# Kernel optimization log

Hardware: AMD Instinct MI355X
Metric: run time of the kernel (lower is better)

The kernel has to match this reference:

```python
import jax, jax.numpy as jnp
import numpy as np

N_EMBD = 1024
N_HEAD = 16
HEAD_DIM = N_EMBD // N_HEAD
LN_EPS = 1e-5


def setup_inputs() -> dict:
    key = jax.random.key(0)
    ks = jax.random.split(key, 8)
    B, T, C = 4, 2048, N_EMBD
    s = lambda fan_in: 1.0 / np.sqrt(fan_in)
    return {
        'x': jax.random.normal(ks[0], (B, T, C), dtype=jnp.float32),
        'w_qkv': jax.random.normal(ks[1], (C, 3 * C), dtype=jnp.float32) * s(C),
        'b_qkv': jnp.zeros((3 * C,), dtype=jnp.float32),
        'ln1_g': jnp.ones((C,), dtype=jnp.float32),
        'ln1_b': jnp.zeros((C,), dtype=jnp.float32),
        'w_fc1': jax.random.normal(ks[2], (C, 4 * C), dtype=jnp.float32) * s(C),
        'b_fc1': jnp.zeros((4 * C,), dtype=jnp.float32),
        'w_fc2': jax.random.normal(ks[3], (4 * C, C), dtype=jnp.float32) * s(4 * C),
        'b_fc2': jnp.zeros((C,), dtype=jnp.float32),
        'ln2_g': jnp.ones((C,), dtype=jnp.float32),
        'ln2_b': jnp.zeros((C,), dtype=jnp.float32),
    }


def _layernorm(x, g, b):
    mu = jnp.mean(x, axis=-1, keepdims=True)
    var = jnp.mean(jnp.square(x - mu), axis=-1, keepdims=True)
    return (x - mu) * jax.lax.rsqrt(var + LN_EPS) * g + b


def _attention(x, w_qkv, b_qkv):
    B, T, C = x.shape
    qkv = x @ w_qkv + b_qkv                      # [B,T,3C]
    q, k, v = jnp.split(qkv, 3, axis=-1)
    q = q.reshape(B, T, N_HEAD, HEAD_DIM)
    k = k.reshape(B, T, N_HEAD, HEAD_DIM)
    v = v.reshape(B, T, N_HEAD, HEAD_DIM)
    scores = jnp.einsum('bqhd,bkhd->bhqk', q, k) / np.sqrt(HEAD_DIM).astype(np.float32)
    causal = jnp.tril(jnp.ones((T, T), dtype=bool))
    scores = jnp.where(causal, scores, -jnp.inf)
    attn = jax.nn.softmax(scores, axis=-1)       # [B,H,T,T]
    y = jnp.einsum('bhqk,bkhd->bqhd', attn, v)
    return y.reshape(B, T, C)


def reference(x, w_qkv, b_qkv, ln1_g, ln1_b, w_fc1, b_fc1, w_fc2, b_fc2, ln2_g, ln2_b):
    # Block: x = ln1(x + attn(x)); x = ln2(x + mlp(x))   (post-LN residual)
    x = _layernorm(x + _attention(x, w_qkv, b_qkv), ln1_g, ln1_b)
    h = jax.nn.gelu(x @ w_fc1 + b_fc1, approximate=False)
    mlp = h @ w_fc2 + b_fc2
    x = _layernorm(x + mlp, ln2_g, ln2_b)
    return x
```

## Files before the change

kernel.cpp:

```cpp
#include <hip/hip_runtime.h>
#include <cstdint>
#include <cstddef>

#define TB 4
#define TT 2048
#define TC 1024
#define NH 16
#define HD 64
#define MROWS (TB * TT)

typedef __bf16 bf16;
typedef unsigned short u16;
typedef __bf16 bf16x8 __attribute__((ext_vector_type(8)));
typedef float floatx4 __attribute__((ext_vector_type(4)));
typedef unsigned short ushort8 __attribute__((ext_vector_type(8)));
typedef unsigned short ushort4v __attribute__((ext_vector_type(4)));

#define LOG2E 1.4426950408889634f

static __device__ __forceinline__ u16 f2bfbits(float f) {
    bf16 b = (bf16)f;
    return __builtin_bit_cast(u16, b);
}

#if __has_builtin(__builtin_amdgcn_exp2f)
#define EXP2F(x) __builtin_amdgcn_exp2f(x)
#else
#define EXP2F(x) exp2f(x)
#endif

static __device__ __forceinline__ void gld_lds16(const u16* g, const u16* lds) {
    __builtin_amdgcn_global_load_lds(
        (const __attribute__((address_space(1))) unsigned int*)(uintptr_t)g,
        (__attribute__((address_space(3))) unsigned int*)(unsigned int)(uintptr_t)lds,
        16, 0, 0);
}

__global__ void cast_bf16_kernel(const float* __restrict__ in, u16* __restrict__ out, int n4) {
    int i = blockIdx.x * blockDim.x + threadIdx.x;
    if (i < n4) {
        float4 v = reinterpret_cast<const float4*>(in)[i];
        ushort4v o;
        o.x = f2bfbits(v.x); o.y = f2bfbits(v.y); o.z = f2bfbits(v.z); o.w = f2bfbits(v.w);
        reinterpret_cast<ushort4v*>(out)[i] = o;
    }
}

__global__ void transpose_cast_kernel(const float* __restrict__ in, u16* __restrict__ out,
                                      int K, int N) {
    __shared__ float tile[32][33];
    const int n0 = blockIdx.x * 32, k0 = blockIdx.y * 32;
    const int tx = threadIdx.x, ty = threadIdx.y;
    for (int r = 0; r < 32; r += 8)
        tile[ty + r][tx] = in[(size_t)(k0 + ty + r) * N + n0 + tx];
    __syncthreads();
    for (int r = 0; r < 32; r += 8)
        out[(size_t)(n0 + ty + r) * K + k0 + tx] = f2bfbits(tile[tx][ty + r]);
}

template <int GELU>
__global__ __launch_bounds__(256) void gemm_bt_kernel(
    const u16* __restrict__ A, const u16* __restrict__ Bt,
    const float* __restrict__ bias, u16* __restrict__ Cmat,
    int Nsz, int Ksz)
{
    __shared__ u16 As[128 * 64];
    __shared__ u16 Bs[128 * 64];
    const int tid  = threadIdx.x;
    const int wave = tid >> 6, lane = tid & 63;
    const int quad = lane >> 4, l16 = lane & 15;
    const int wm = (wave >> 1) * 64, wn = (wave & 1) * 64;
    const int m0 = blockIdx.y * 128, n0 = blockIdx.x * 128;

    const int srow = lane >> 3;
    const int scol = ((lane & 7) ^ srow) * 8;
    const u16* ap = A  + (size_t)(m0 + wave * 32 + srow) * Ksz + scol;
    const u16* bp = Bt + (size_t)(n0 + wave * 32 + srow) * Ksz + scol;
    const size_t dstep = (size_t)8 * Ksz;

    floatx4 acc[4][4];
#pragma unroll
    for (int i = 0; i < 4; i++)
#pragma unroll
        for (int j = 0; j < 4; j++)
            acc[i][j] = (floatx4){0.f, 0.f, 0.f, 0.f};

    const int l7 = l16 & 7;

    for (int k0 = 0; k0 < Ksz; k0 += 64) {
        __syncthreads();
#pragma unroll
        for (int d = 0; d < 4; d++) {
            gld_lds16(ap + d * dstep, As + (wave * 4 + d) * 512);
            gld_lds16(bp + d * dstep, Bs + (wave * 4 + d) * 512);
        }
        ap += 64; bp += 64;
        __syncthreads();

#pragma unroll
        for (int t = 0; t < 2; t++) {
            const int po = ((t * 4 + quad) ^ l7) * 8;
            bf16x8 af[4], bfr[4];
#pragma unroll
            for (int i = 0; i < 4; i++)
                af[i] = *reinterpret_cast<const bf16x8*>(As + (wm + i * 16 + l16) * 64 + po);
#pragma unroll
            for (int j = 0; j < 4; j++)
                bfr[j] = *reinterpret_cast<const bf16x8*>(Bs + (wn + j * 16 + l16) * 64 + po);
#pragma unroll
            for (int i = 0; i < 4; i++)
#pragma unroll
                for (int j = 0; j < 4; j++)
                    acc[i][j] = __builtin_amdgcn_mfma_f32_16x16x32_bf16(af[i], bfr[j], acc[i][j], 0, 0, 0);
        }
    }

#pragma unroll
    for (int i = 0; i < 4; i++) {
        const int row_base = m0 + wm + i * 16 + quad * 4;
#pragma unroll
        for (int j = 0; j < 4; j++) {
            const int col = n0 + wn + j * 16 + l16;
            const float bv = bias[col];
#pragma unroll
            for (int r = 0; r < 4; r++) {
                float v = acc[i][j][r] + bv;
                if (GELU) {
                    float u = v * (0.7978845608f + 0.0356774081f * v * v);
                    float e = EXP2F(u * (2.0f * LOG2E));
                    v = v - v * __builtin_amdgcn_rcpf(e + 1.0f);
                }
                Cmat[(size_t)(row_base + r) * Nsz + col] = f2bfbits(v);
            }
        }
    }
}

__global__ __launch_bounds__(256, 4) void attn_kernel(const u16* __restrict__ qkv,
                                                      u16* __restrict__ y)
{
    __shared__ u16 Ks[64 * 64];
    __shared__ u16 Vt[64 * 64];
    __shared__ u16 Pw[4][16 * 64];
    const int tid  = threadIdx.x;
    const int wave = tid >> 6, lane = tid & 63;
    const int quad = lane >> 4, l16 = lane & 15;
    const int l7   = l16 & 7;
    const int h = blockIdx.y, b = blockIdx.z;
    const int rowbase = b * TT;
    const int S3C = 3 * TC;

    const int srow = tid >> 3;
    const int kc8  = (tid & 7) * 8;
    const int pcK  = ((tid & 7) ^ (srow & 7)) * 8;
    const int pvb  = (srow + ((tid & 7) << 2)) & 31;
    const int pcr  = (quad ^ l7) * 8;
    unsigned int* const vtw = (unsigned int*)Vt;
    const int wavq = wave * 16 + l16;

    for (int pass = 0; pass < 2; pass++) {
        const int qt  = pass ? (31 - (int)blockIdx.x) : (int)blockIdx.x;
        const int q0b = qt * 64;
        const int q0w = q0b + wave * 16;
        const int kend = q0b + 64;

        bf16x8 qf0, qf1;
        {
            const u16* qrow = qkv + (size_t)(rowbase + q0w + l16) * S3C + h * HD + quad * 8;
            bf16x8 t0 = *reinterpret_cast<const bf16x8*>(qrow);
            bf16x8 t1 = *reinterpret_cast<const bf16x8*>(qrow + 32);
#pragma unroll
            for (int i = 0; i < 8; i++) {
                t0[i] = (bf16)((float)t0[i] * (0.125f * LOG2E));
                t1[i] = (bf16)((float)t1[i] * (0.125f * LOG2E));
            }
            qf0 = t0; qf1 = t1;
        }

        float m_s = -__builtin_inff(), l_s = 0.f;
        floatx4 o_acc[4];
#pragma unroll
        for (int n = 0; n < 4; n++) o_acc[n] = (floatx4){0.f, 0.f, 0.f, 0.f};

        ushort8 kr0, kr1, vr0, vr1;
        {
            const u16* kb = qkv + (size_t)(rowbase + srow) * S3C + TC + h * HD + kc8;
            kr0 = *reinterpret_cast<const ushort8*>(kb);
            kr1 = *reinterpret_cast<const ushort8*>(kb + (size_t)32 * S3C);
            const u16* vb = qkv + (size_t)(rowbase + 2 * srow) * S3C + 2 * TC + h * HD + kc8;
            vr0 = *reinterpret_cast<const ushort8*>(vb);
            vr1 = *reinterpret_cast<const ushort8*>(vb + S3C);
        }

        for (int k0 = 0; k0 < kend; k0 += 64) {
            __syncthreads();
            *reinterpret_cast<ushort8*>(Ks + srow * 64 + pcK)        = kr0;
            *reinterpret_cast<ushort8*>(Ks + (srow + 32) * 64 + pcK) = kr1;
#pragma unroll
            for (int j = 0; j < 8; j++) {
                unsigned int pk = (unsigned int)vr0[j] | ((unsigned int)vr1[j] << 16);
                vtw[(kc8 + j) * 32 + (pvb ^ (j << 2))] = pk;
            }
            __syncthreads();

            if (k0 + 64 < kend) {
                const int kn = k0 + 64;
                const u16* kb = qkv + (size_t)(rowbase + kn + srow) * S3C + TC + h * HD + kc8;
                kr0 = *reinterpret_cast<const ushort8*>(kb);
                kr1 = *reinterpret_cast<const ushort8*>(kb + (size_t)32 * S3C);
                const u16* vb = qkv + (size_t)(rowbase + kn + 2 * srow) * S3C + 2 * TC + h * HD + kc8;
                vr0 = *reinterpret_cast<const ushort8*>(vb);
                vr1 = *reinterpret_cast<const ushort8*>(vb + S3C);
            }

            floatx4 st[4];
#pragma unroll
            for (int t = 0; t < 4; t++) {
                const u16* krowp = Ks + (t * 16 + l16) * 64;
                bf16x8 ka  = *reinterpret_cast<const bf16x8*>(krowp + pcr);
                bf16x8 kb2 = *reinterpret_cast<const bf16x8*>(krowp + (pcr ^ 32));
                floatx4 s = (floatx4){0.f, 0.f, 0.f, 0.f};
                s = __builtin_amdgcn_mfma_f32_16x16x32_bf16(ka, qf0, s, 0, 0, 0);
                s = __builtin_amdgcn_mfma_f32_16x16x32_bf16(kb2, qf1, s, 0, 0, 0);
                st[t] = s;
            }
            float v[16];
            if (k0 == q0b) {
#pragma unroll
                for (int t = 0; t < 4; t++)
#pragma unroll
                    for (int r = 0; r < 4; r++)
                        v[t * 4 + r] = (t * 16 + quad * 4 + r > wavq) ? -__builtin_inff()
                                                                      : st[t][r];
            } else {
#pragma unroll
                for (int t = 0; t < 4; t++)
#pragma unroll
                    for (int r = 0; r < 4; r++)
                        v[t * 4 + r] = st[t][r];
            }
            float mx = v[0];
#pragma unroll
            for (int i = 1; i < 16; i++) mx = fmaxf(mx, v[i]);
            mx = fmaxf(mx, __shfl_xor(mx, 16));
            mx = fmaxf(mx, __shfl_xor(mx, 32));
            const float mnew  = fmaxf(m_s, mx);
            const float alpha = EXP2F(m_s - mnew);
            float rs = 0.f;
            u16* const pwb = Pw[wave] + l16 * 64;
#pragma unroll
            for (int t = 0; t < 4; t++) {
                float p0 = EXP2F(v[t * 4 + 0] - mnew);
                float p1 = EXP2F(v[t * 4 + 1] - mnew);
                float p2 = EXP2F(v[t * 4 + 2] - mnew);
                float p3 = EXP2F(v[t * 4 + 3] - mnew);
                rs += (p0 + p1) + (p2 + p3);
                ushort4v pk;
                pk.x = f2bfbits(p0); pk.y = f2bfbits(p1);
                pk.z = f2bfbits(p2); pk.w = f2bfbits(p3);
                *reinterpret_cast<ushort4v*>(
                    pwb + ((2 * t + (quad >> 1)) ^ l7) * 8 + (quad & 1) * 4) = pk;
            }
            rs += __shfl_xor(rs, 16);
            rs += __shfl_xor(rs, 32);
            l_s = l_s * alpha + rs;
            m_s = mnew;
#pragma unroll
            for (int n = 0; n < 4; n++) o_acc[n] *= alpha;

            bf16x8 pf0 = *reinterpret_cast<const bf16x8*>(pwb + pcr);
            bf16x8 pf1 = *reinterpret_cast<const bf16x8*>(pwb + (pcr ^ 32));
#pragma unroll
            for (int n = 0; n < 4; n++) {
                const int dr  = n * 16 + l16;
                const int pd0 = ((4 * (quad + 2 * n + (l16 >> 3))) & 31) ^ (l7 << 2);
                bf16x8 vf0 = *reinterpret_cast<const bf16x8*>(vtw + dr * 32 + pd0);
                bf16x8 vf1 = *reinterpret_cast<const bf16x8*>(vtw + dr * 32 + (pd0 ^ 16));
                o_acc[n] = __builtin_amdgcn_mfma_f32_16x16x32_bf16(vf0, pf0, o_acc[n], 0, 0, 0);
                o_acc[n] = __builtin_amdgcn_mfma_f32_16x16x32_bf16(vf1, pf1, o_acc[n], 0, 0, 0);
            }
        }

        const float li = 1.0f / l_s;
        u16* yrow = y + (size_t)(rowbase + q0w + l16) * TC + h * HD;
#pragma unroll
        for (int n = 0; n < 4; n++) {
            ushort4v ov;
            ov.x = f2bfbits(o_acc[n][0] * li);
            ov.y = f2bfbits(o_acc[n][1] * li);
            ov.z = f2bfbits(o_acc[n][2] * li);
            ov.w = f2bfbits(o_acc[n][3] * li);
            *reinterpret_cast<ushort4v*>(yrow + n * 16 + quad * 4) = ov;
        }
    }
}

template <typename AT, typename OT>
__global__ __launch_bounds__(256) void ln_kernel(
    const AT* __restrict__ a, const bf16* __restrict__ bres,
    const float* __restrict__ g, const float* __restrict__ be,
    OT* __restrict__ out)
{
    const int row = blockIdx.x;
    const int tid = threadIdx.x;
    const size_t base = (size_t)row * TC;
    float v[4];
    for (int i = 0; i < 4; i++) {
        const int c = tid + i * 256;
        v[i] = (float)a[base + c] + (float)bres[base + c];
    }
    float s  = v[0] + v[1] + v[2] + v[3];
    float sq = v[0]*v[0] + v[1]*v[1] + v[2]*v[2] + v[3]*v[3];
    for (int off = 32; off >= 1; off >>= 1) {
        s  += __shfl_xor(s, off, 64);
        sq += __shfl_xor(sq, off, 64);
    }
    __shared__ float red[8];
    const int wv = tid >> 6, lane = tid & 63;
    if (lane == 0) { red[wv] = s; red[4 + wv] = sq; }
    __syncthreads();
    s  = red[0] + red[1] + red[2] + red[3];
    sq = red[4] + red[5] + red[6] + red[7];
    const float mu   = s * (1.0f / TC);
    const float var  = sq * (1.0f / TC) - mu * mu;
    const float rsig = rsqrtf(var + 1e-5f);
    for (int i = 0; i < 4; i++) {
        const int c = tid + i * 256;
        out[base + c] = (OT)((v[i] - mu) * rsig * g[c] + be[c]);
    }
}

extern "C" void kernel_launch(void* const* d_in, const int* in_sizes, int n_in,
                              void* d_out, int out_size, void* d_ws, size_t ws_size,
                              hipStream_t stream)
{
    const float* x     = (const float*)d_in[0];
    const float* w_qkv = (const float*)d_in[1];
    const float* b_qkv = (const float*)d_in[2];
    const float* ln1_g = (const float*)d_in[3];
    const float* ln1_b = (const float*)d_in[4];
    const float* w_fc1 = (const float*)d_in[5];
    const float* b_fc1 = (const float*)d_in[6];
    const float* w_fc2 = (const float*)d_in[7];
    const float* b_fc2 = (const float*)d_in[8];
    const float* ln2_g = (const float*)d_in[9];
    const float* ln2_b = (const float*)d_in[10];
    float* out = (float*)d_out;

    char* ws = (char*)d_ws;
    const size_t MB = 1ull << 20;
    u16* xb    = (u16*)(ws + 0);
    u16* wqkvT = (u16*)(ws + 16 * MB);
    u16* wfc1T = (u16*)(ws + 22 * MB);
    u16* wfc2T = (u16*)(ws + 30 * MB);
    u16* qkv   = (u16*)(ws + 38 * MB);
    u16* yb    = (u16*)(ws + 86 * MB);
    u16* x1    = (u16*)(ws + 102 * MB);
    u16* hb    = (u16*)(ws + 118 * MB);
    u16* mlp   = (u16*)(ws + 38 * MB);

    cast_bf16_kernel<<<(MROWS * TC / 4 + 255) / 256, 256, 0, stream>>>(x, xb, MROWS * TC / 4);
    transpose_cast_kernel<<<dim3(3 * TC / 32, TC / 32), dim3(32, 8), 0, stream>>>(w_qkv, wqkvT, TC, 3 * TC);
    transpose_cast_kernel<<<dim3(4 * TC / 32, TC / 32), dim3(32, 8), 0, stream>>>(w_fc1, wfc1T, TC, 4 * TC);
    transpose_cast_kernel<<<dim3(TC / 32, 4 * TC / 32), dim3(32, 8), 0, stream>>>(w_fc2, wfc2T, 4 * TC, TC);

    gemm_bt_kernel<0><<<dim3(3 * TC / 128, MROWS / 128), 256, 0, stream>>>(
        xb, wqkvT, b_qkv, qkv, 3 * TC, TC);
    attn_kernel<<<dim3(16, NH, TB), 256, 0, stream>>>(qkv, yb);
    ln_kernel<float, bf16><<<MROWS, 256, 0, stream>>>(x, (const bf16*)yb, ln1_g, ln1_b, (bf16*)x1);
    gemm_bt_kernel<1><<<dim3(4 * TC / 128, MROWS / 128), 256, 0, stream>>>(
        (const u16*)x1, wfc1T, b_fc1, hb, 4 * TC, TC);
    gemm_bt_kernel<0><<<dim3(TC / 128, MROWS / 128), 256, 0, stream>>>(
        hb, wfc2T, b_fc2, mlp, TC, 4 * TC);
    ln_kernel<bf16, float><<<MROWS, 256, 0, stream>>>(
        (const bf16*)x1, (const bf16*)mlp, ln2_g, ln2_b, out);
}
```

Before: 495.5 us.

## Merge prep kernels, pack GEMM epilogue stores, double-buffer 128-row attention tiles

Four cast/transpose launches are merged into one prep kernel that dispatches on block index. The GEMM epilogue now exchanges values between lane pairs so each lane writes packed 32-bit bf16 pairs instead of scalar 16-bit stores. The attention kernel moves to 512 threads covering 128 query rows, with double-buffered K/V in LDS, one barrier per step, and separate thread halves for the K and V staging. Waves skip fully masked key tiles. The tradeoff is more LDS and fewer blocks, and waves in the same block do unequal amounts of causal work.

```diff
diff --git a/kernel.cpp b/kernel.cpp
--- a/kernel.cpp
+++ b/kernel.cpp
@@ -36,21 +36,30 @@
         16, 0, 0);
 }
 
-__global__ void cast_bf16_kernel(const float* __restrict__ in, u16* __restrict__ out, int n4) {
-    int i = blockIdx.x * blockDim.x + threadIdx.x;
-    if (i < n4) {
-        float4 v = reinterpret_cast<const float4*>(in)[i];
+__global__ __launch_bounds__(256) void prep_kernel(
+    const float* __restrict__ x, u16* __restrict__ xb,
+    const float* __restrict__ w_qkv, u16* __restrict__ wqkvT,
+    const float* __restrict__ w_fc1, u16* __restrict__ wfc1T,
+    const float* __restrict__ w_fc2, u16* __restrict__ wfc2T)
+{
+    const int tid = threadIdx.x;
+    int blk = blockIdx.x;
+    if (blk < 8192) {
+        const int i = blk * 256 + tid;
+        float4 v = reinterpret_cast<const float4*>(x)[i];
         ushort4v o;
         o.x = f2bfbits(v.x); o.y = f2bfbits(v.y); o.z = f2bfbits(v.z); o.w = f2bfbits(v.w);
-        reinterpret_cast<ushort4v*>(out)[i] = o;
-    }
-}
-
-__global__ void transpose_cast_kernel(const float* __restrict__ in, u16* __restrict__ out,
-                                      int K, int N) {
+        reinterpret_cast<ushort4v*>(xb)[i] = o;
+        return;
+    }
+    blk -= 8192;
+    const float* in; u16* out; int K, N, bx, by;
+    if (blk < 3072)      { in = w_qkv; out = wqkvT; K = TC;     N = 3 * TC; bx = blk % 96;  by = blk / 96; }
+    else if (blk < 7168) { blk -= 3072; in = w_fc1; out = wfc1T; K = TC;    N = 4 * TC; bx = blk & 127; by = blk >> 7; }
+    else                 { blk -= 7168; in = w_fc2; out = wfc2T; K = 4 * TC; N = TC;    bx = blk & 31;  by = blk >> 5; }
     __shared__ float tile[32][33];
-    const int n0 = blockIdx.x * 32, k0 = blockIdx.y * 32;
-    const int tx = threadIdx.x, ty = threadIdx.y;
+    const int n0 = bx * 32, k0 = by * 32;
+    const int tx = tid & 31, ty = tid >> 5;
     for (int r = 0; r < 32; r += 8)
         tile[ty + r][tx] = in[(size_t)(k0 + ty + r) * N + n0 + tx];
     __syncthreads();
@@ -115,33 +124,48 @@
         }
     }
 
+    float bv[4];
+#pragma unroll
+    for (int j = 0; j < 4; j++) bv[j] = bias[n0 + wn + j * 16 + l16];
+    const int odd = l16 & 1;
 #pragma unroll
     for (int i = 0; i < 4; i++) {
-        const int row_base = m0 + wm + i * 16 + quad * 4;
+        const int row0 = m0 + wm + i * 16 + quad * 4;
 #pragma unroll
         for (int j = 0; j < 4; j++) {
-            const int col = n0 + wn + j * 16 + l16;
-            const float bv = bias[col];
+            float v[4];
 #pragma unroll
             for (int r = 0; r < 4; r++) {
-                float v = acc[i][j][r] + bv;
+                float t = acc[i][j][r] + bv[j];
                 if (GELU) {
-                    float u = v * (0.7978845608f + 0.0356774081f * v * v);
+                    float u = t * (0.7978845608f + 0.0356774081f * t * t);
                     float e = EXP2F(u * (2.0f * LOG2E));
-                    v = v - v * __builtin_amdgcn_rcpf(e + 1.0f);
-                }
-                Cmat[(size_t)(row_base + r) * Nsz + col] = f2bfbits(v);
+                    t = t - t * __builtin_amdgcn_rcpf(e + 1.0f);
+                }
+                v[r] = t;
             }
-        }
-    }
-}
-
-__global__ __launch_bounds__(256, 4) void attn_kernel(const u16* __restrict__ qkv,
-                                                      u16* __restrict__ y)
+            float pv0 = __shfl_xor(v[0], 1), pv1 = __shfl_xor(v[1], 1);
+            float pv2 = __shfl_xor(v[2], 1), pv3 = __shfl_xor(v[3], 1);
+            float lo0 = odd ? pv2 : v[0];
+            float hi0 = odd ? v[2] : pv0;
+            float lo1 = odd ? pv3 : v[1];
+            float hi1 = odd ? v[3] : pv1;
+            unsigned int d0 = (unsigned int)f2bfbits(lo0) | ((unsigned int)f2bfbits(hi0) << 16);
+            unsigned int d1 = (unsigned int)f2bfbits(lo1) | ((unsigned int)f2bfbits(hi1) << 16);
+            const int row  = row0 + odd * 2;
+            const int colp = n0 + wn + j * 16 + (l16 & ~1);
+            *reinterpret_cast<unsigned int*>(Cmat + (size_t)row * Nsz + colp)       = d0;
+            *reinterpret_cast<unsigned int*>(Cmat + (size_t)(row + 1) * Nsz + colp) = d1;
+        }
+    }
+}
+
+__global__ __launch_bounds__(512) void attn_kernel(const u16* __restrict__ qkv,
+                                                   u16* __restrict__ y)
 {
-    __shared__ u16 Ks[64 * 64];
-    __shared__ u16 Vt[64 * 64];
-    __shared__ u16 Pw[4][16 * 64];
+    __shared__ u16 Ks[2 * 64 * 64];
+    __shared__ u16 Vt[2 * 64 * 64];
+    __shared__ u16 Pw[8][16 * 64];
     const int tid  = threadIdx.x;
     const int wave = tid >> 6, lane = tid & 63;
     const int quad = lane >> 4, l16 = lane & 15;
@@ -150,19 +174,21 @@
     const int rowbase = b * TT;
     const int S3C = 3 * TC;
 
-    const int srow = tid >> 3;
-    const int kc8  = (tid & 7) * 8;
+    const int srow = (tid >> 3) & 31;
+    const int c8   = (tid & 7) * 8;
     const int pcK  = ((tid & 7) ^ (srow & 7)) * 8;
     const int pvb  = (srow + ((tid & 7) << 2)) & 31;
-    const int pcr  = (quad ^ l7) * 8;
+    const bool kRole = (tid < 256);
+    const int pcr = (quad ^ l7) * 8;
     unsigned int* const vtw = (unsigned int*)Vt;
-    const int wavq = wave * 16 + l16;
 
     for (int pass = 0; pass < 2; pass++) {
-        const int qt  = pass ? (31 - (int)blockIdx.x) : (int)blockIdx.x;
-        const int q0b = qt * 64;
-        const int q0w = q0b + wave * 16;
-        const int kend = q0b + 64;
+        const int qt   = pass ? (15 - (int)blockIdx.x) : (int)blockIdx.x;
+        const int q0b  = qt * 128;
+        const int q0w  = q0b + wave * 16;
+        const int kend = q0b + 128;
+
+        __syncthreads();
 
         bf16x8 qf0, qf1;
         {
@@ -182,103 +208,107 @@
 #pragma unroll
         for (int n = 0; n < 4; n++) o_acc[n] = (floatx4){0.f, 0.f, 0.f, 0.f};
 
-        ushort8 kr0, kr1, vr0, vr1;
-        {
-            const u16* kb = qkv + (size_t)(rowbase + srow) * S3C + TC + h * HD + kc8;
-            kr0 = *reinterpret_cast<const ushort8*>(kb);
-            kr1 = *reinterpret_cast<const ushort8*>(kb + (size_t)32 * S3C);
-            const u16* vb = qkv + (size_t)(rowbase + 2 * srow) * S3C + 2 * TC + h * HD + kc8;
-            vr0 = *reinterpret_cast<const ushort8*>(vb);
-            vr1 = *reinterpret_cast<const ushort8*>(vb + S3C);
-        }
-
+        const u16* gp = kRole
+            ? qkv + (size_t)(rowbase + srow) * S3C + TC + h * HD + c8
+            : qkv + (size_t)(rowbase + 2 * srow) * S3C + 2 * TC + h * HD + c8;
+        const size_t g2 = kRole ? (size_t)32 * S3C : (size_t)S3C;
+        ushort8 r0 = *reinterpret_cast<const ushort8*>(gp);
+        ushort8 r1 = *reinterpret_cast<const ushort8*>(gp + g2);
+
+        int buf = 0;
         for (int k0 = 0; k0 < kend; k0 += 64) {
-            __syncthreads();
-            *reinterpret_cast<ushort8*>(Ks + srow * 64 + pcK)        = kr0;
-            *reinterpret_cast<ushort8*>(Ks + (srow + 32) * 64 + pcK) = kr1;
-#pragma unroll
-            for (int j = 0; j < 8; j++) {
-                unsigned int pk = (unsigned int)vr0[j] | ((unsigned int)vr1[j] << 16);
-                vtw[(kc8 + j) * 32 + (pvb ^ (j << 2))] = pk;
+            if (kRole) {
+                u16* kb = Ks + buf * 4096;
+                *reinterpret_cast<ushort8*>(kb + srow * 64 + pcK)        = r0;
+                *reinterpret_cast<ushort8*>(kb + (srow + 32) * 64 + pcK) = r1;
+            } else {
+                unsigned int* vb = vtw + buf * 2048;
+#pragma unroll
+                for (int j = 0; j < 8; j++) {
+                    unsigned int pk = (unsigned int)r0[j] | ((unsigned int)r1[j] << 16);
+                    vb[(c8 + j) * 32 + (pvb ^ (j << 2))] = pk;
+                }
             }
             __syncthreads();
 
             if (k0 + 64 < kend) {
-                const int kn = k0 + 64;
-                const u16* kb = qkv + (size_t)(rowbase + kn + srow) * S3C + TC + h * HD + kc8;
-                kr0 = *reinterpret_cast<const ushort8*>(kb);
-                kr1 = *reinterpret_cast<const ushort8*>(kb + (size_t)32 * S3C);
-                const u16* vb = qkv + (size_t)(rowbase + kn + 2 * srow) * S3C + 2 * TC + h * HD + kc8;
-                vr0 = *reinterpret_cast<const ushort8*>(vb);
-                vr1 = *reinterpret_cast<const ushort8*>(vb + S3C);
+                const u16* gn = gp + (size_t)(k0 + 64) * S3C;
+                r0 = *reinterpret_cast<const ushort8*>(gn);
+                r1 = *reinterpret_cast<const ushort8*>(gn + g2);
             }
 
-            floatx4 st[4];
-#pragma unroll
-            for (int t = 0; t < 4; t++) {
-                const u16* krowp = Ks + (t * 16 + l16) * 64;
-                bf16x8 ka  = *reinterpret_cast<const bf16x8*>(krowp + pcr);
-                bf16x8 kb2 = *reinterpret_cast<const bf16x8*>(krowp + (pcr ^ 32));
-                floatx4 s = (floatx4){0.f, 0.f, 0.f, 0.f};
-                s = __builtin_amdgcn_mfma_f32_16x16x32_bf16(ka, qf0, s, 0, 0, 0);
-                s = __builtin_amdgcn_mfma_f32_16x16x32_bf16(kb2, qf1, s, 0, 0, 0);
-                st[t] = s;
+            if (k0 <= q0w + 15) {
+                const u16* ksb = Ks + buf * 4096;
+                floatx4 st[4];
+#pragma unroll
+                for (int t = 0; t < 4; t++) {
+                    const u16* krowp = ksb + (t * 16 + l16) * 64;
+                    bf16x8 ka  = *reinterpret_cast<const bf16x8*>(krowp + pcr);
+                    bf16x8 kb2 = *reinterpret_cast<const bf16x8*>(krowp + (pcr ^ 32));
+                    floatx4 s = (floatx4){0.f, 0.f, 0.f, 0.f};
+                    s = __builtin_amdgcn_mfma_f32_16x16x32_bf16(ka, qf0, s, 0, 0, 0);
+                    s = __builtin_amdgcn_mfma_f32_16x16x32_bf16(kb2, qf1, s, 0, 0, 0);
+                    st[t] = s;
+                }
+                float v[16];
+                if (k0 + 63 > q0w) {
+                    const int kq = k0 - q0w;
+#pragma unroll
+                    for (int t = 0; t < 4; t++)
+#pragma unroll
+                        for (int r = 0; r < 4; r++)
+                            v[t * 4 + r] = (t * 16 + quad * 4 + r + kq > l16)
+                                               ? -__builtin_inff() : st[t][r];
+                } else {
+#pragma unroll
+                    for (int t = 0; t < 4; t++)
+#pragma unroll
+                        for (int r = 0; r < 4; r++)
+                            v[t * 4 + r] = st[t][r];
+                }
+                float mx = v[0];
+#pragma unroll
+                for (int i = 1; i < 16; i++) mx = fmaxf(mx, v[i]);
+                mx = fmaxf(mx, __shfl_xor(mx, 16));
+                mx = fmaxf(mx, __shfl_xor(mx, 32));
+                const float mnew  = fmaxf(m_s, mx);
+                const float alpha = EXP2F(m_s - mnew);
+                float rs = 0.f;
+                u16* const pwb = Pw[wave] + l16 * 64;
+#pragma unroll
+                for (int t = 0; t < 4; t++) {
+                    float p0 = EXP2F(v[t * 4 + 0] - mnew);
+                    float p1 = EXP2F(v[t * 4 + 1] - mnew);
+                    float p2 = EXP2F(v[t * 4 + 2] - mnew);
+                    float p3 = EXP2F(v[t * 4 + 3] - mnew);
+                    rs += (p0 + p1) + (p2 + p3);
+                    ushort4v pk;
+                    pk.x = f2bfbits(p0); pk.y = f2bfbits(p1);
+                    pk.z = f2bfbits(p2); pk.w = f2bfbits(p3);
+                    *reinterpret_cast<ushort4v*>(
+                        pwb + ((2 * t + (quad >> 1)) ^ l7) * 8 + (quad & 1) * 4) = pk;
+                }
+                rs += __shfl_xor(rs, 16);
+                rs += __shfl_xor(rs, 32);
+                l_s = l_s * alpha + rs;
+                m_s = mnew;
+#pragma unroll
+                for (int n = 0; n < 4; n++) o_acc[n] *= alpha;
+
+                bf16x8 pf0 = *reinterpret_cast<const bf16x8*>(pwb + pcr);
+                bf16x8 pf1 = *reinterpret_cast<const bf16x8*>(pwb + (pcr ^ 32));
+                const unsigned int* vbb = vtw + buf * 2048;
+#pragma unroll
+                for (int n = 0; n < 4; n++) {
+                    const int dr  = n * 16 + l16;
+                    const int pd0 = ((4 * (quad + 2 * n + (l16 >> 3))) & 31) ^ (l7 << 2);
+                    bf16x8 vf0 = *reinterpret_cast<const bf16x8*>(vbb + dr * 32 + pd0);
+                    bf16x8 vf1 = *reinterpret_cast<const bf16x8*>(vbb + dr * 32 + (pd0 ^ 16));
+                    o_acc[n] = __builtin_amdgcn_mfma_f32_16x16x32_bf16(vf0, pf0, o_acc[n], 0, 0, 0);
+                    o_acc[n] = __builtin_amdgcn_mfma_f32_16x16x32_bf16(vf1, pf1, o_acc[n], 0, 0, 0);
+                }
             }
-            float v[16];
-            if (k0 == q0b) {
-#pragma unroll
-                for (int t = 0; t < 4; t++)
-#pragma unroll
-                    for (int r = 0; r < 4; r++)
-                        v[t * 4 + r] = (t * 16 + quad * 4 + r > wavq) ? -__builtin_inff()
-                                                                      : st[t][r];
-            } else {
-#pragma unroll
-                for (int t = 0; t < 4; t++)
-#pragma unroll
-                    for (int r = 0; r < 4; r++)
-                        v[t * 4 + r] = st[t][r];
-            }
-            float mx = v[0];
-#pragma unroll
-            for (int i = 1; i < 16; i++) mx = fmaxf(mx, v[i]);
-            mx = fmaxf(mx, __shfl_xor(mx, 16));
-            mx = fmaxf(mx, __shfl_xor(mx, 32));
-            const float mnew  = fmaxf(m_s, mx);
-            const float alpha = EXP2F(m_s - mnew);
-            float rs = 0.f;
-            u16* const pwb = Pw[wave] + l16 * 64;
-#pragma unroll
-            for (int t = 0; t < 4; t++) {
-                float p0 = EXP2F(v[t * 4 + 0] - mnew);
-                float p1 = EXP2F(v[t * 4 + 1] - mnew);
-                float p2 = EXP2F(v[t * 4 + 2] - mnew);
-                float p3 = EXP2F(v[t * 4 + 3] - mnew);
-                rs += (p0 + p1) + (p2 + p3);
-                ushort4v pk;
-                pk.x = f2bfbits(p0); pk.y = f2bfbits(p1);
-                pk.z = f2bfbits(p2); pk.w = f2bfbits(p3);
-                *reinterpret_cast<ushort4v*>(
-                    pwb + ((2 * t + (quad >> 1)) ^ l7) * 8 + (quad & 1) * 4) = pk;
-            }
-            rs += __shfl_xor(rs, 16);
-            rs += __shfl_xor(rs, 32);
-            l_s = l_s * alpha + rs;
-            m_s = mnew;
-#pragma unroll
-            for (int n = 0; n < 4; n++) o_acc[n] *= alpha;
-
-            bf16x8 pf0 = *reinterpret_cast<const bf16x8*>(pwb + pcr);
-            bf16x8 pf1 = *reinterpret_cast<const bf16x8*>(pwb + (pcr ^ 32));
-#pragma unroll
-            for (int n = 0; n < 4; n++) {
-                const int dr  = n * 16 + l16;
-                const int pd0 = ((4 * (quad + 2 * n + (l16 >> 3))) & 31) ^ (l7 << 2);
-                bf16x8 vf0 = *reinterpret_cast<const bf16x8*>(vtw + dr * 32 + pd0);
-                bf16x8 vf1 = *reinterpret_cast<const bf16x8*>(vtw + dr * 32 + (pd0 ^ 16));
-                o_acc[n] = __builtin_amdgcn_mfma_f32_16x16x32_bf16(vf0, pf0, o_acc[n], 0, 0, 0);
-                o_acc[n] = __builtin_amdgcn_mfma_f32_16x16x32_bf16(vf1, pf1, o_acc[n], 0, 0, 0);
-            }
+            buf ^= 1;
         }
 
         const float li = 1.0f / l_s;
@@ -359,14 +389,11 @@
     u16* hb    = (u16*)(ws + 118 * MB);
     u16* mlp   = (u16*)(ws + 38 * MB);
 
-    cast_bf16_kernel<<<(MROWS * TC / 4 + 255) / 256, 256, 0, stream>>>(x, xb, MROWS * TC / 4);
-    transpose_cast_kernel<<<dim3(3 * TC / 32, TC / 32), dim3(32, 8), 0, stream>>>(w_qkv, wqkvT, TC, 3 * TC);
-    transpose_cast_kernel<<<dim3(4 * TC / 32, TC / 32), dim3(32, 8), 0, stream>>>(w_fc1, wfc1T, TC, 4 * TC);
-    transpose_cast_kernel<<<dim3(TC / 32, 4 * TC / 32), dim3(32, 8), 0, stream>>>(w_fc2, wfc2T, 4 * TC, TC);
+    prep_kernel<<<19456, 256, 0, stream>>>(x, xb, w_qkv, wqkvT, w_fc1, wfc1T, w_fc2, wfc2T);
 
     gemm_bt_kernel<0><<<dim3(3 * TC / 128, MROWS / 128), 256, 0, stream>>>(
         xb, wqkvT, b_qkv, qkv, 3 * TC, TC);
-    attn_kernel<<<dim3(16, NH, TB), 256, 0, stream>>>(qkv, yb);
+    attn_kernel<<<dim3(8, NH, TB), 512, 0, stream>>>(qkv, yb);
     ln_kernel<float, bf16><<<MROWS, 256, 0, stream>>>(x, (const bf16*)yb, ln1_g, ln1_b, (bf16*)x1);
     gemm_bt_kernel<1><<<dim3(4 * TC / 128, MROWS / 128), 256, 0, stream>>>(
         (const u16*)x1, wfc1T, b_fc1, hb, 4 * TC, TC);
```

After: 465.4 us. -6.1%, faster.
